# Optimization experiments

Measured on AMD Instinct MI355X. Metric: run time of the kernel, lower is better.

## Reference

```python
import jax, jax.numpy as jnp
import numpy as np

# ---- constants from module defaults ----
IMG, PS, STRIDE, C_IN = 224, 16, 8, 1
NP1D = (IMG - PS) // STRIDE + 1          # 27
NUM_PATCHES = NP1D * NP1D                # 729
EMBED = 64
N_INPUT = NUM_PATCHES * EMBED            # 46656
N_HIDDEN = 1000                          # d_model
N_RNN = 100
N_STEPS = 5
BETA, THR = 0.8, 0.5
BETA_R, THR_R = 0.95, 1.0
LM_SPN = 0.0058
ALPHA = 2.0  # snntorch ATan surrogate default

@jax.custom_vjp
def spike(x):
    return (x > 0).astype(x.dtype)

def _spike_fwd(x):
    return spike(x), x

def _spike_bwd(x, g):
    # snntorch ATan surrogate gradient
    return (g * (ALPHA / 2.0) / (1.0 + (jnp.pi / 2.0 * ALPHA * x) ** 2),)

spike.defvjp(_spike_fwd, _spike_bwd)

def extract_patches(x):
    # x: [B, C, H, W] -> [B, num_patches, C*PS*PS] matching torch unfold+permute+flatten
    B, C, H, W = x.shape
    idx = (jnp.arange(NP1D)[:, None] * STRIDE + jnp.arange(PS)).reshape(-1)  # [NP1D*PS]
    t = x[:, :, idx, :].reshape(B, C, NP1D, PS, W)
    t = t[..., idx].reshape(B, C, NP1D, PS, NP1D, PS)
    t = t.transpose(0, 2, 4, 1, 3, 5)  # [B, nh, nw, C, ph, pw]
    return t.reshape(B, NUM_PATCHES, C * PS * PS)

def setup_inputs() -> dict:
    key = jax.random.key(0)
    ks = jax.random.split(key, 12)
    def lin(k, fi, fo):
        kw, kb = jax.random.split(k)
        s = 1.0 / np.sqrt(fi)
        return (jax.random.uniform(kw, (fi, fo), jnp.float32, -s, s),
                jax.random.uniform(kb, (fo,), jnp.float32, -s, s))
    W_pe, b_pe = lin(ks[0], C_IN * PS * PS, EMBED)
    pos_embed = 0.02 * jax.random.normal(ks[1], (1, NUM_PATCHES, EMBED), jnp.float32)
    W1, b1 = lin(ks[2], N_INPUT, N_HIDDEN)
    W2, b2 = lin(ks[3], N_HIDDEN, N_HIDDEN)
    W3, b3 = lin(ks[4], N_HIDDEN, N_HIDDEN)
    WR, bR = lin(ks[5], N_HIDDEN, N_RNN)
    Vw, Vb = lin(ks[6], N_RNN, N_RNN)      # RLeaky recurrent linear
    Wq, bq = lin(ks[7], N_RNN, N_HIDDEN)
    Wk, bk = lin(ks[8], N_HIDDEN, N_HIDDEN)
    Wv, bv = lin(ks[9], N_HIDDEN, N_HIDDEN)
    Wo, bo = lin(ks[10], N_HIDDEN, 1)       # cross_last=True -> output_proj to 1
    data = jax.random.normal(ks[11], (32, C_IN, IMG, IMG), jnp.float32)
    return {"data": data, "W_pe": W_pe, "b_pe": b_pe, "pos_embed": pos_embed,
            "W1": W1, "b1": b1, "W2": W2, "b2": b2, "W3": W3, "b3": b3,
            "WR": WR, "bR": bR, "Vw": Vw, "Vb": Vb,
            "Wq": Wq, "bq": bq, "Wk": Wk, "bk": bk, "Wv": Wv, "bv": bv,
            "Wo": Wo, "bo": bo}

def _forward(data, W_pe, b_pe, pos_embed, W1, b1, W2, b2, W3, b3,
             WR, bR, Vw, Vb, Wq, bq, Wk, bk, Wv, bv, Wo, bo):
    B = data.shape[0]
    patches = extract_patches(data)                      # [B, 729, 256]
    x = patches @ W_pe + b_pe + pos_embed               # [B, 729, 64]
    x_flat = x.reshape(B, -1)                            # [B, 46656]
    cur1 = x_flat @ W1 + b1                              # constant across steps
    scale = jnp.sqrt(jnp.asarray(N_HIDDEN, jnp.float32))  # head_dim = d_model (1 head)

    def leaky(mem, cur, beta=BETA, thr=THR):
        reset = jax.lax.stop_gradient(spike(mem - thr))
        mem = beta * mem + cur - reset * thr
        return mem, spike(mem - thr)

    def step(carry, t):
        mem1, mem2, mem3, spk_r, mem_r, mem_out, total, prev, reg = carry
        # layers[:2] call -- first Leaky1 update
        mem1, spk1 = leaky(mem1, cur1)
        # layers[:7] call -- Leaky1 state updated a SECOND time (same x_flat)
        mem1, spk1b = leaky(mem1, cur1)
        mem2, spk2 = leaky(mem2, spk1b @ W2 + b2)
        mem3, spk3 = leaky(mem3, spk2 @ W3 + b3)  # Dropout is identity in eval
        total = total + spk1.mean() + spk3.mean()
        # RLeaky (beta=0.95, threshold=1.0, subtract reset, recurrent linear)
        rlin = spk1 @ WR + bR
        reset_r = jax.lax.stop_gradient(spike(mem_r - THR_R))
        mem_r = BETA_R * mem_r + rlin + spk_r @ Vw + Vb - reset_r * THR_R
        spk_r = spike(mem_r - THR_R)
        total = total + spk_r.mean()
        # cross-attention: feature dim acts as the sequence dim (seq=1 in view)
        q = spk_r @ Wq + bq                               # [B, 1000]
        k = spk3 @ Wk + bk                                # [B, 1000]
        v = spk3 @ Wv + bv                                # [B, 1000]
        probs = jax.nn.softmax(q[:, :, None] * k[:, None, :] / scale, axis=-1)  # [B,1000,1000]
        att = jnp.einsum('bij,bj->bi', probs, v) @ Wo + bo  # [B, 1]
        mem_out, spk_out = leaky(mem_out, att)
        mem_out = jax.lax.stop_gradient(mem_out)          # .detach() in source
        total = total + spk_out.mean()
        reg = reg + LM_SPN * total + jnp.where(t > 0, LM_SPN * jnp.abs(total - prev), 0.0)
        return (mem1, mem2, mem3, spk_r, mem_r, mem_out, total, total, reg), spk_out

    z = jnp.float32(0.0)
    init = (jnp.zeros((B, N_HIDDEN)), jnp.zeros((B, N_HIDDEN)), jnp.zeros((B, N_HIDDEN)),
            jnp.zeros((B, N_RNN)), jnp.zeros((B, N_RNN)), jnp.zeros((B, 1)), z, z, z)
    carry, spk_rec = jax.lax.scan(step, init, jnp.arange(N_STEPS))
    out = spk_rec.sum(0)[:, 0] / N_STEPS                  # [B]
    reg_norm = carry[-1] / N_STEPS
    return out, reg_norm

def reference(data, W_pe, b_pe, pos_embed, W1, b1, W2, b2, W3, b3,
              WR, bR, Vw, Vb, Wq, bq, Wk, bk, Wv, bv, Wo, bo):
    return _forward(data, W_pe, b_pe, pos_embed, W1, b1, W2, b2, W3, b3,
                    WR, bR, Vw, Vb, Wq, bq, Wk, bk, Wv, bv, Wo, bo)
```

## Files before the change

### kernel.cpp

```cpp
#include <hip/hip_runtime.h>

#define OFF_X     0
#define OFF_CUR1  1492992
#define OFF_MEM1  1524992
#define OFF_MEM2  1556992
#define OFF_MEM3  1588992
#define OFF_SPK1B 1652992
#define OFF_MEMR  1844992
#define OFF_SPKR  1848192
#define OFF_MEMO  1851392
#define OFF_PATT  1851424
#define OFF_CNT   1851680
#define OFF_OACC  1851700
#define OFF_SC    1851732
#define OFF_TICK  1851736
#define OFF_PART  1851744
#define OFF_PG2   OFF_PART
#define OFF_PG3   (OFF_PART + 800000)
#define OFF_PKK   (OFF_PART + 1600000)
#define OFF_PVV   (OFF_PART + 2400000)
#define OFF_M2B   (OFF_PART + 3200000)
#define OFF_M3B   (OFF_PART + 3232000)

static constexpr float kBETA  = 0.8f;
static constexpr float kTHR   = 0.5f;
static constexpr float kBETAR = 0.95f;
static constexpr float kTHRR  = 1.0f;
static constexpr float kLM    = 0.0058f;

__global__ void k_init(float* ws) {
    int idx = blockIdx.x * 256 + threadIdx.x;
    if (idx < 96000) {
        ws[OFF_MEM1 + idx] = 0.f;
    } else {
        int j = idx - 96000;
        if (j < 6752) ws[OFF_MEMR + j] = 0.f;
    }
}

__global__ __launch_bounds__(64) void k_patch(
    const float* __restrict__ data, const float* __restrict__ Wpe,
    const float* __restrict__ bpe, const float* __restrict__ pos,
    float* __restrict__ xf)
{
    int b = blockIdx.x, pr = blockIdx.y;
    int tid = threadIdx.x;
    const float* db = data + (size_t)b * 50176 + pr * 1792;
    float bb = bpe[tid];
    float acc[27];
    #pragma unroll
    for (int pc = 0; pc < 27; ++pc)
        acc[pc] = bb + pos[(pr * 27 + pc) * 64 + tid];
    #pragma unroll 2
    for (int c = 0; c < 256; ++c) {
        float w = Wpe[c * 64 + tid];
        const float* row = db + (c >> 4) * 224 + (c & 15);
        #pragma unroll
        for (int pc = 0; pc < 27; ++pc)
            acc[pc] = fmaf(row[pc * 8], w, acc[pc]);
    }
    size_t obase = (size_t)b * 46656 + (size_t)pr * 27 * 64 + tid;
    #pragma unroll
    for (int pc = 0; pc < 27; ++pc)
        xf[obase + (size_t)pc * 64] = acc[pc];
}

__global__ __launch_bounds__(256) void k_gemm1_part(
    const float* __restrict__ xf, const float* __restrict__ W1,
    float* __restrict__ part, int tpc)
{
    int chunk = blockIdx.x;
    int hg = blockIdx.y;
    int t0 = chunk * tpc;
    int t1 = t0 + tpc; if (t1 > 729) t1 = 729;
    int tid = threadIdx.x;
    __shared__ float xs[2048];
    float acc[32][2];
    #pragma unroll
    for (int b = 0; b < 32; ++b) { acc[b][0] = 0.f; acc[b][1] = 0.f; }

    const int hbase = hg * 500;
    const bool ok1 = (tid + 256) < 500;
    const int h0 = hbase + tid;
    const int h1 = hbase + (ok1 ? tid + 256 : 0);
    for (int tt = t0; tt < t1; ++tt) {
        int i0 = tt * 64;
        __syncthreads();
        for (int l = tid; l < 2048; l += 256)
            xs[l] = xf[(size_t)(l >> 6) * 46656 + i0 + (l & 63)];
        __syncthreads();
        for (int ii4 = 0; ii4 < 16; ++ii4) {
            int i = i0 + ii4 * 4;
            const float* c0 = W1 + (size_t)i * 1000 + h0;
            const float* c1 = W1 + (size_t)i * 1000 + h1;
            float w0a = c0[0], w1a = c0[1000], w2a = c0[2000], w3a = c0[3000];
            float w0b = ok1 ? c1[0]    : 0.f;
            float w1b = ok1 ? c1[1000] : 0.f;
            float w2b = ok1 ? c1[2000] : 0.f;
            float w3b = ok1 ? c1[3000] : 0.f;
            #pragma unroll
            for (int b = 0; b < 32; ++b) {
                float4 xv = *reinterpret_cast<const float4*>(&xs[b * 64 + ii4 * 4]);
                float a0 = acc[b][0], a1 = acc[b][1];
                a0 = fmaf(xv.x, w0a, a0);  a1 = fmaf(xv.x, w0b, a1);
                a0 = fmaf(xv.y, w1a, a0);  a1 = fmaf(xv.y, w1b, a1);
                a0 = fmaf(xv.z, w2a, a0);  a1 = fmaf(xv.z, w2b, a1);
                a0 = fmaf(xv.w, w3a, a0);  a1 = fmaf(xv.w, w3b, a1);
                acc[b][0] = a0; acc[b][1] = a1;
            }
        }
    }
    float* pc = part + (size_t)chunk * 32000 + hbase;
    #pragma unroll
    for (int b = 0; b < 32; ++b) {
        pc[b * 1000 + tid] = acc[b][0];
        if (ok1) pc[b * 1000 + tid + 256] = acc[b][1];
    }
}

__global__ void k_gemm1_reduce(const float* __restrict__ part,
                               const float* __restrict__ b1,
                               float* __restrict__ cur1, int nchunk)
{
    int idx = blockIdx.x * 128 + threadIdx.x;
    if (idx >= 32000) return;
    int h = idx % 1000;
    float a0 = b1[h], a1 = 0.f, a2 = 0.f, a3 = 0.f;
    int c = 0;
    for (; c + 4 <= nchunk; c += 4) {
        a0 += part[(size_t)c * 32000 + idx];
        a1 += part[(size_t)(c + 1) * 32000 + idx];
        a2 += part[(size_t)(c + 2) * 32000 + idx];
        a3 += part[(size_t)(c + 3) * 32000 + idx];
    }
    for (; c < nchunk; ++c) a0 += part[(size_t)c * 32000 + idx];
    cur1[idx] = (a0 + a1) + (a2 + a3);
}

__global__ __launch_bounds__(512) void k_stepR(
    const float* __restrict__ cur1, float* __restrict__ mem1,
    float* __restrict__ spk1b,
    const float* __restrict__ WR, const float* __restrict__ bR,
    const float* __restrict__ Vw, const float* __restrict__ Vb,
    float* __restrict__ mem_r, float* __restrict__ spk_r,
    float* cnt0, float* cnt2)
{
    int b = blockIdx.x;
    int tid = threadIdx.x;
    __shared__ float s1[1000];
    __shared__ float sr[100];
    __shared__ float red2[4][128];
    __shared__ float csum[8];

    float localc = 0.f;
    if (tid < 250) {
        int base = b * 1000 + tid * 4;
        float4 m4 = *reinterpret_cast<const float4*>(&mem1[base]);
        float4 c4 = *reinterpret_cast<const float4*>(&cur1[base]);
        float mm[4] = {m4.x, m4.y, m4.z, m4.w};
        float cc[4] = {c4.x, c4.y, c4.z, c4.w};
        float mb[4], sb[4];
        #pragma unroll
        for (int q = 0; q < 4; ++q) {
            float m = mm[q], c = cc[q];
            float r1 = (m - kTHR > 0.f) ? kTHR : 0.f;
            float ma = __fsub_rn(__fadd_rn(__fmul_rn(kBETA, m), c), r1);
            float s  = (ma - kTHR > 0.f) ? 1.f : 0.f;
            float r2 = __fmul_rn(s, kTHR);
            float mv = __fsub_rn(__fadd_rn(__fmul_rn(kBETA, ma), c), r2);
            sb[q] = (mv - kTHR > 0.f) ? 1.f : 0.f;
            mb[q] = mv;
            s1[tid * 4 + q] = s;
            localc += s;
        }
        *reinterpret_cast<float4*>(&mem1[base])  = make_float4(mb[0], mb[1], mb[2], mb[3]);
        *reinterpret_cast<float4*>(&spk1b[base]) = make_float4(sb[0], sb[1], sb[2], sb[3]);
    }
    if (tid < 100) sr[tid] = spk_r[b * 100 + tid];
    for (int off = 32; off; off >>= 1) localc += __shfl_down(localc, off, 64);
    if ((tid & 63) == 0) csum[tid >> 6] = localc;
    __syncthreads();
    if (tid == 0) {
        float cs = 0.f;
        #pragma unroll
        for (int w = 0; w < 8; ++w) cs += csum[w];
        atomicAdd(cnt0, cs);
    }

    int ks = tid >> 7, hh = tid & 127;
    float p = 0.f;
    if (hh < 100) {
        const float* wp = WR + (size_t)(ks * 250) * 100 + hh;
        int j0 = ks * 250;
        #pragma unroll 5
        for (int j = 0; j < 250; ++j) p = fmaf(s1[j0 + j], wp[(size_t)j * 100], p);
    }
    red2[ks][hh] = p;
    __syncthreads();
    float s = 0.f;
    if (tid < 100) {
        float acc = bR[tid] + ((red2[0][tid] + red2[1][tid]) + (red2[2][tid] + red2[3][tid]));
        float rec = 0.f;
        for (int j = 0; j < 100; ++j) rec = fmaf(sr[j], Vw[j * 100 + tid], rec);
        float m = mem_r[b * 100 + tid];
        float r = (m - kTHRR > 0.f) ? kTHRR : 0.f;
        float mn = __fsub_rn(__fadd_rn(__fadd_rn(__fadd_rn(__fmul_rn(kBETAR, m), acc), rec), Vb[tid]), r);
        s = (mn - kTHRR > 0.f) ? 1.f : 0.f;
        mem_r[b * 100 + tid] = mn;
        spk_r[b * 100 + tid] = s;
    }
    unsigned long long msk = __ballot(s > 0.5f);
    if ((tid & 63) == 0) {
        int pc2 = __popcll(msk);
        if (pc2) atomicAdd(cnt2, (float)pc2);
    }
}

__global__ __launch_bounds__(256) void k_gsp(
    const float* __restrict__ A, const float* __restrict__ W,
    float* __restrict__ part)
{
    int hb = blockIdx.x, kc = blockIdx.y, bg = blockIdx.z;
    int tid = threadIdx.x;
    int j0 = kc * 40;
    __shared__ __align__(16) float al[320];
    __shared__ float redg[8 * 128];
    for (int l = tid; l < 320; l += 256)
        al[l] = A[(size_t)(bg * 8 + (l & 7)) * 1000 + j0 + (l >> 3)];
    __syncthreads();
    int ks = tid >> 7, hh = tid & 127;
    float acc[8];
    #pragma unroll
    for (int b = 0; b < 8; ++b) acc[b] = 0.f;
    if (hh < 125) {
        int h = hb * 125 + hh;
        const float* Wp = W + (size_t)(j0 + ks * 20) * 1000 + h;
        const float4* abase = reinterpret_cast<const float4*>(&al[ks * 20 * 8]);
        #pragma unroll 4
        for (int jj = 0; jj < 20; ++jj) {
            float w = Wp[(size_t)jj * 1000];
            const float4* a4 = abase + jj * 2;
            #pragma unroll
            for (int q = 0; q < 2; ++q) {
                float4 av = a4[q];
                acc[q * 4 + 0] = fmaf(av.x, w, acc[q * 4 + 0]);
                acc[q * 4 + 1] = fmaf(av.y, w, acc[q * 4 + 1]);
                acc[q * 4 + 2] = fmaf(av.z, w, acc[q * 4 + 2]);
                acc[q * 4 + 3] = fmaf(av.w, w, acc[q * 4 + 3]);
            }
        }
    }
    if (ks == 1 && hh < 125) {
        #pragma unroll
        for (int b = 0; b < 8; ++b) redg[b * 128 + hh] = acc[b];
    }
    __syncthreads();
    if (ks == 0 && hh < 125) {
        int h = hb * 125 + hh;
        float* pp = part + (size_t)kc * 32000 + (size_t)(bg * 8) * 1000 + h;
        #pragma unroll
        for (int b = 0; b < 8; ++b) pp[(size_t)b * 1000] = acc[b] + redg[b * 128 + hh];
    }
}

template <bool COUNT>
__global__ __launch_bounds__(256) void k_gspred(
    const float* __restrict__ pin, const float* __restrict__ bias,
    const float* __restrict__ mem_old, float* __restrict__ mem_new,
    const float* __restrict__ W, float* __restrict__ pout, float* cnt)
{
    int hs = blockIdx.x, kc = blockIdx.y, bg = blockIdx.z;
    int tid = threadIdx.x;
    int j0 = kc * 40;
    __shared__ __align__(16) float al[320];
    __shared__ float redg[8 * 128];
    __shared__ float csum[4];
    float localc = 0.f;
    for (int e = tid; e < 320; e += 256) {
        int jj = e % 40, bi = e / 40;
        int idx = (bg * 8 + bi) * 1000 + j0 + jj;
        float a = bias[j0 + jj];
        #pragma unroll 5
        for (int c = 0; c < 25; ++c) a += pin[(size_t)c * 32000 + idx];
        float m = mem_old[idx];
        float r = (m - kTHR > 0.f) ? kTHR : 0.f;
        float mn = __fsub_rn(__fadd_rn(__fmul_rn(kBETA, m), a), r);
        float s = (mn - kTHR > 0.f) ? 1.f : 0.f;
        al[jj * 8 + bi] = s;
        if (hs == 0) { mem_new[idx] = mn; localc += s; }
    }
    if (COUNT) {
        for (int off = 32; off; off >>= 1) localc += __shfl_down(localc, off, 64);
        if ((tid & 63) == 0) csum[tid >> 6] = localc;
    }
    __syncthreads();
    if (COUNT && tid == 0 && hs == 0) {
        float tot = csum[0] + csum[1] + csum[2] + csum[3];
        if (tot != 0.f) atomicAdd(cnt, tot);
    }
    int ks = tid >> 7, hh = tid & 127;
    float acc[8];
    #pragma unroll
    for (int b = 0; b < 8; ++b) acc[b] = 0.f;
    if (hh < 125) {
        int h = hs * 125 + hh;
        const float* Wp = W + (size_t)(j0 + ks * 20) * 1000 + h;
        const float4* abase = reinterpret_cast<const float4*>(&al[ks * 20 * 8]);
        #pragma unroll 4
        for (int jj = 0; jj < 20; ++jj) {
            float w = Wp[(size_t)jj * 1000];
            const float4* a4 = abase + jj * 2;
            #pragma unroll
            for (int q = 0; q < 2; ++q) {
                float4 av = a4[q];
                acc[q * 4 + 0] = fmaf(av.x, w, acc[q * 4 + 0]);
                acc[q * 4 + 1] = fmaf(av.y, w, acc[q * 4 + 1]);
                acc[q * 4 + 2] = fmaf(av.z, w, acc[q * 4 + 2]);
                acc[q * 4 + 3] = fmaf(av.w, w, acc[q * 4 + 3]);
            }
        }
    }
    if (ks == 1 && hh < 125) {
        #pragma unroll
        for (int b = 0; b < 8; ++b) redg[b * 128 + hh] = acc[b];
    }
    __syncthreads();
    if (ks == 0 && hh < 125) {
        int h = hs * 125 + hh;
        float* pp = pout + (size_t)kc * 32000 + (size_t)(bg * 8) * 1000 + h;
        #pragma unroll
        for (int b = 0; b < 8; ++b) pp[(size_t)b * 1000] = acc[b] + redg[b * 128 + hh];
    }
}

__global__ __launch_bounds__(256) void k_gspred_kv(
    const float* __restrict__ pin, const float* __restrict__ bias,
    const float* __restrict__ mem_old, float* __restrict__ mem_new,
    const float* __restrict__ Wk, const float* __restrict__ Wv,
    float* __restrict__ pk, float* __restrict__ pv, float* cnt)
{
    int hs = blockIdx.x, kc = blockIdx.y, bg = blockIdx.z;
    int tid = threadIdx.x;
    int j0 = kc * 40;
    __shared__ __align__(16) float al[320];
    __shared__ float redk[8 * 128];
    __shared__ float redv[8 * 128];
    __shared__ float csum[4];
    float localc = 0.f;
    for (int e = tid; e < 320; e += 256) {
        int jj = e % 40, bi = e / 40;
        int idx = (bg * 8 + bi) * 1000 + j0 + jj;
        float a = bias[j0 + jj];
        #pragma unroll 5
        for (int c = 0; c < 25; ++c) a += pin[(size_t)c * 32000 + idx];
        float m = mem_old[idx];
        float r = (m - kTHR > 0.f) ? kTHR : 0.f;
        float mn = __fsub_rn(__fadd_rn(__fmul_rn(kBETA, m), a), r);
        float s = (mn - kTHR > 0.f) ? 1.f : 0.f;
        al[jj * 8 + bi] = s;
        if (hs == 0) { mem_new[idx] = mn; localc += s; }
    }
    for (int off = 32; off; off >>= 1) localc += __shfl_down(localc, off, 64);
    if ((tid & 63) == 0) csum[tid >> 6] = localc;
    __syncthreads();
    if (tid == 0 && hs == 0) {
        float tot = csum[0] + csum[1] + csum[2] + csum[3];
        if (tot != 0.f) atomicAdd(cnt, tot);
    }
    int ks = tid >> 7, hh = tid & 127;
    float ak[8], av2[8];
    #pragma unroll
    for (int b = 0; b < 8; ++b) { ak[b] = 0.f; av2[b] = 0.f; }
    if (hh < 125) {
        int h = hs * 125 + hh;
        const float* wkp = Wk + (size_t)(j0 + ks * 20) * 1000 + h;
        const float* wvp = Wv + (size_t)(j0 + ks * 20) * 1000 + h;
        const float4* abase = reinterpret_cast<const float4*>(&al[ks * 20 * 8]);
        #pragma unroll 4
        for (int jj = 0; jj < 20; ++jj) {
            float wk = wkp[(size_t)jj * 1000];
            float wv = wvp[(size_t)jj * 1000];
            const float4* a4 = abase + jj * 2;
            #pragma unroll
            for (int q = 0; q < 2; ++q) {
                float4 av = a4[q];
                ak[q * 4 + 0] = fmaf(av.x, wk, ak[q * 4 + 0]);
                ak[q * 4 + 1] = fmaf(av.y, wk, ak[q * 4 + 1]);
                ak[q * 4 + 2] = fmaf(av.z, wk, ak[q * 4 + 2]);
                ak[q * 4 + 3] = fmaf(av.w, wk, ak[q * 4 + 3]);
                av2[q * 4 + 0] = fmaf(av.x, wv, av2[q * 4 + 0]);
                av2[q * 4 + 1] = fmaf(av.y, wv, av2[q * 4 + 1]);
                av2[q * 4 + 2] = fmaf(av.z, wv, av2[q * 4 + 2]);
                av2[q * 4 + 3] = fmaf(av.w, wv, av2[q * 4 + 3]);
            }
        }
    }
    if (ks == 1 && hh < 125) {
        #pragma unroll
        for (int b = 0; b < 8; ++b) { redk[b * 128 + hh] = ak[b]; redv[b * 128 + hh] = av2[b]; }
    }
    __syncthreads();
    if (ks == 0 && hh < 125) {
        int h = hs * 125 + hh;
        float* ppk = pk + (size_t)kc * 32000 + (size_t)(bg * 8) * 1000 + h;
        float* ppv = pv + (size_t)kc * 32000 + (size_t)(bg * 8) * 1000 + h;
        #pragma unroll
        for (int b = 0; b < 8; ++b) {
            ppk[(size_t)b * 1000] = ak[b] + redk[b * 128 + hh];
            ppv[(size_t)b * 1000] = av2[b] + redv[b * 128 + hh];
        }
    }
}

__global__ __launch_bounds__(256) void k_attnred(
    const float* __restrict__ pkk, const float* __restrict__ pvv,
    const float* __restrict__ bk, const float* __restrict__ bv,
    const float* __restrict__ spkr, const float* __restrict__ Wq,
    const float* __restrict__ bq, const float* __restrict__ Wo,
    const float* __restrict__ bo,
    float* __restrict__ patt, float* __restrict__ memo,
    float* __restrict__ oacc, const float* __restrict__ cnt,
    float* __restrict__ sc, float* __restrict__ dout,
    unsigned int* __restrict__ tick, int t)
{
    int it = blockIdx.x, b = blockIdx.y;
    int tid = threadIdx.x;
    __shared__ float kk[1000], vv[1000];
    __shared__ float sr[100];
    __shared__ float red[256];
    __shared__ float pden[256], pnum[256];
    __shared__ int isLast;
    float pmax = -3.4e38f, pmin = 3.4e38f;
    if (tid < 100) sr[tid] = spkr[b * 100 + tid];
    for (int h = tid; h < 1000; h += 256) {
        int idx = b * 1000 + h;
        float ak = bk[h], av = bv[h];
        #pragma unroll 5
        for (int c = 0; c < 25; ++c) {
            ak += pkk[(size_t)c * 32000 + idx];
            av += pvv[(size_t)c * 32000 + idx];
        }
        kk[h] = ak; vv[h] = av;
        pmax = fmaxf(pmax, ak);
        pmin = fminf(pmin, ak);
    }
    red[tid] = pmax;
    __syncthreads();
    for (int s2 = 128; s2 > 0; s2 >>= 1) {
        if (tid < s2) red[tid] = fmaxf(red[tid], red[tid + s2]);
        __syncthreads();
    }
    float kmax = red[0];
    __syncthreads();
    red[tid] = pmin;
    __syncthreads();
    for (int s2 = 128; s2 > 0; s2 >>= 1) {
        if (tid < s2) red[tid] = fminf(red[tid], red[tid + s2]);
        __syncthreads();
    }
    float kmin = red[0];
    __syncthreads();

    int half = tid >> 7, lane = tid & 127;
    float den = 0.f, num = 0.f;
    if (lane < 125) {
        int i = it * 125 + lane;
        float qi = bq[i];
        for (int j = 0; j < 100; ++j) qi = fmaf(sr[j], Wq[j * 1000 + i], qi);
        float qs = qi / 31.62277660168379f;
        float m = (qs >= 0.f) ? qs * kmax : qs * kmin;
        int jb = half * 500;
        for (int j = 0; j < 500; ++j) {
            float e = __expf(fmaf(qs, kk[jb + j], -m));
            den += e;
            num = fmaf(e, vv[jb + j], num);
        }
    }
    pden[tid] = den; pnum[tid] = num;
    __syncthreads();
    float pw = 0.f;
    if (tid < 125) {
        float dsum = pden[tid] + pden[tid + 128];
        float nsum = pnum[tid] + pnum[tid + 128];
        pw = (nsum / dsum) * Wo[it * 125 + tid];
    }
    red[tid] = (tid < 125) ? pw : 0.f;
    __syncthreads();
    for (int s2 = 128; s2 > 0; s2 >>= 1) {
        if (tid < s2) red[tid] += red[tid + s2];
        __syncthreads();
    }
    if (tid == 0) patt[b * 8 + it] = red[0];
    __syncthreads();
    if (tid == 0) {
        __threadfence();
        unsigned r = atomicAdd(tick, 1u);
        isLast = (r == 255u) ? 1 : 0;
    }
    __syncthreads();
    if (isLast && tid < 64) {
        __threadfence();
        float s = 0.f;
        if (tid < 32) {
            float a = bo[0];
            for (int itx = 0; itx < 8; ++itx) a += patt[tid * 8 + itx];
            float m = memo[tid];
            float r = (m - kTHR > 0.f) ? kTHR : 0.f;
            float mn = __fsub_rn(__fadd_rn(__fmul_rn(kBETA, m), a), r);
            memo[tid] = mn;
            s = (mn - kTHR > 0.f) ? 1.f : 0.f;
            float oa = oacc[tid] + s;
            oacc[tid] = oa;
            if (t == 4) dout[tid] = oa / 5.0f;
        }
        unsigned long long msk = __ballot(s > 0.5f);
        float co = (float)__popcll(msk);
        if (tid == 0) {
            float total = sc[0];
            float prev = total;
            total = __fadd_rn(total, __fdiv_rn(cnt[0], 32000.f));
            total = __fadd_rn(total, __fdiv_rn(cnt[1], 32000.f));
            total = __fadd_rn(total, __fdiv_rn(cnt[2], 3200.f));
            total = __fadd_rn(total, __fdiv_rn(co, 32.f));
            float reg = sc[1];
            reg = __fadd_rn(reg, __fmul_rn(kLM, total));
            if (t > 0) reg = __fadd_rn(reg, __fmul_rn(kLM, fabsf(__fsub_rn(total, prev))));
            sc[0] = total; sc[1] = reg;
            if (t == 4) dout[32] = reg / 5.0f;
        }
    }
}

extern "C" void kernel_launch(void* const* d_in, const int* in_sizes, int n_in,
                              void* d_out, int out_size, void* d_ws, size_t ws_size,
                              hipStream_t stream)
{
    const float* data = (const float*)d_in[0];
    const float* Wpe  = (const float*)d_in[1];
    const float* bpe  = (const float*)d_in[2];
    const float* pos  = (const float*)d_in[3];
    const float* W1   = (const float*)d_in[4];
    const float* b1   = (const float*)d_in[5];
    const float* W2   = (const float*)d_in[6];
    const float* b2   = (const float*)d_in[7];
    const float* W3   = (const float*)d_in[8];
    const float* b3   = (const float*)d_in[9];
    const float* WR   = (const float*)d_in[10];
    const float* bR   = (const float*)d_in[11];
    const float* Vw   = (const float*)d_in[12];
    const float* Vb   = (const float*)d_in[13];
    const float* Wq   = (const float*)d_in[14];
    const float* bq   = (const float*)d_in[15];
    const float* Wk   = (const float*)d_in[16];
    const float* bk   = (const float*)d_in[17];
    const float* Wv   = (const float*)d_in[18];
    const float* bv   = (const float*)d_in[19];
    const float* Wo   = (const float*)d_in[20];
    const float* bo   = (const float*)d_in[21];

    float* ws = (float*)d_ws;
    float* dout = (float*)d_out;

    float* xf    = ws + OFF_X;
    float* cur1  = ws + OFF_CUR1;
    float* mem1  = ws + OFF_MEM1;
    float* mem2a = ws + OFF_MEM2;
    float* mem3a = ws + OFF_MEM3;
    float* spk1b = ws + OFF_SPK1B;
    float* memr  = ws + OFF_MEMR;
    float* spkr  = ws + OFF_SPKR;
    float* memo  = ws + OFF_MEMO;
    float* patt  = ws + OFF_PATT;
    float* cntb  = ws + OFF_CNT;
    float* oacc  = ws + OFF_OACC;
    float* sc    = ws + OFF_SC;
    unsigned int* tick = (unsigned int*)(ws + OFF_TICK);
    float* part  = ws + OFF_PART;
    float* pg2   = ws + OFF_PG2;
    float* pg3   = ws + OFF_PG3;
    float* pkk   = ws + OFF_PKK;
    float* pvv   = ws + OFF_PVV;
    float* mem2b = ws + OFF_M2B;
    float* mem3b = ws + OFF_M3B;

    size_t ws_f = ws_size / 4;
    size_t avail = (ws_f > OFF_PART) ? (ws_f - OFF_PART) : 0;
    long nchunk_l = (long)(avail / 32000);
    int nchunk = (nchunk_l > 365) ? 365 : (int)nchunk_l;
    if (nchunk < 1) nchunk = 1;
    int tpc = (729 + nchunk - 1) / nchunk;
    nchunk = (729 + tpc - 1) / tpc;

    k_init<<<402, 256, 0, stream>>>(ws);
    k_patch<<<dim3(32, 27), 64, 0, stream>>>(data, Wpe, bpe, pos, xf);
    k_gemm1_part<<<dim3(nchunk, 2), 256, 0, stream>>>(xf, W1, part, tpc);
    k_gemm1_reduce<<<250, 128, 0, stream>>>(part, b1, cur1, nchunk);

    for (int t = 0; t < 5; ++t) {
        float* cnt = cntb + t * 4;
        float* m2o = (t & 1) ? mem2b : mem2a;
        float* m2n = (t & 1) ? mem2a : mem2b;
        float* m3o = (t & 1) ? mem3b : mem3a;
        float* m3n = (t & 1) ? mem3a : mem3b;

        k_stepR<<<32, 512, 0, stream>>>(cur1, mem1, spk1b, WR, bR, Vw, Vb,
                                        memr, spkr, cnt + 0, cnt + 2);
        k_gsp<<<dim3(8, 25, 4), 256, 0, stream>>>(spk1b, W2, pg2);
        k_gspred<false><<<dim3(8, 25, 4), 256, 0, stream>>>(
            pg2, b2, m2o, m2n, W3, pg3, nullptr);
        k_gspred_kv<<<dim3(8, 25, 4), 256, 0, stream>>>(
            pg3, b3, m3o, m3n, Wk, Wv, pkk, pvv, cnt + 1);
        k_attnred<<<dim3(8, 32), 256, 0, stream>>>(
            pkk, pvv, bk, bv, spkr, Wq, bq, Wo, bo,
            patt, memo, oacc, cnt, sc, dout, tick + t, t);
    }
    (void)in_sizes; (void)n_in; (void)out_size;
}
```

Baseline: 545.1 us.

## Fold per-step leaky update and RNN layer into neighboring kernels to cut launches

Removes the separate k_stepR launch each timestep. The layer-1 membrane update for the next step now runs in extra blocks of k_attnred, with one initial k_stepA launch before the loop. The RLeaky recurrent layer runs in an extra block column of k_gsp. This trims five serial launches and lets small work overlap with the larger kernels. The cost is an extra spike buffer, added branch divergence and resource pressure in both host kernels, and a dependence on spk_r being read in k_attnred before k_gsp of the next step updates it.

```diff
diff --git a/kernel.cpp b/kernel.cpp
--- a/kernel.cpp
+++ b/kernel.cpp
@@ -21,6 +21,7 @@
 #define OFF_PVV   (OFF_PART + 2400000)
 #define OFF_M2B   (OFF_PART + 3200000)
 #define OFF_M3B   (OFF_PART + 3232000)
+#define OFF_SPK1  (OFF_PART + 3264000)
 
 static constexpr float kBETA  = 0.8f;
 static constexpr float kTHR   = 0.5f;
@@ -137,94 +138,87 @@
     cur1[idx] = (a0 + a1) + (a2 + a3);
 }
 
-__global__ __launch_bounds__(512) void k_stepR(
-    const float* __restrict__ cur1, float* __restrict__ mem1,
-    float* __restrict__ spk1b,
-    const float* __restrict__ WR, const float* __restrict__ bR,
-    const float* __restrict__ Vw, const float* __restrict__ Vb,
-    float* __restrict__ mem_r, float* __restrict__ spk_r,
-    float* cnt0, float* cnt2)
-{
-    int b = blockIdx.x;
-    int tid = threadIdx.x;
-    __shared__ float s1[1000];
-    __shared__ float sr[100];
-    __shared__ float red2[4][128];
-    __shared__ float csum[8];
-
-    float localc = 0.f;
-    if (tid < 250) {
-        int base = b * 1000 + tid * 4;
-        float4 m4 = *reinterpret_cast<const float4*>(&mem1[base]);
-        float4 c4 = *reinterpret_cast<const float4*>(&cur1[base]);
-        float mm[4] = {m4.x, m4.y, m4.z, m4.w};
-        float cc[4] = {c4.x, c4.y, c4.z, c4.w};
-        float mb[4], sb[4];
-        #pragma unroll
-        for (int q = 0; q < 4; ++q) {
-            float m = mm[q], c = cc[q];
-            float r1 = (m - kTHR > 0.f) ? kTHR : 0.f;
-            float ma = __fsub_rn(__fadd_rn(__fmul_rn(kBETA, m), c), r1);
-            float s  = (ma - kTHR > 0.f) ? 1.f : 0.f;
-            float r2 = __fmul_rn(s, kTHR);
-            float mv = __fsub_rn(__fadd_rn(__fmul_rn(kBETA, ma), c), r2);
-            sb[q] = (mv - kTHR > 0.f) ? 1.f : 0.f;
-            mb[q] = mv;
-            s1[tid * 4 + q] = s;
-            localc += s;
-        }
-        *reinterpret_cast<float4*>(&mem1[base])  = make_float4(mb[0], mb[1], mb[2], mb[3]);
-        *reinterpret_cast<float4*>(&spk1b[base]) = make_float4(sb[0], sb[1], sb[2], sb[3]);
-    }
-    if (tid < 100) sr[tid] = spk_r[b * 100 + tid];
-    for (int off = 32; off; off >>= 1) localc += __shfl_down(localc, off, 64);
-    if ((tid & 63) == 0) csum[tid >> 6] = localc;
-    __syncthreads();
-    if (tid == 0) {
-        float cs = 0.f;
-        #pragma unroll
-        for (int w = 0; w < 8; ++w) cs += csum[w];
-        atomicAdd(cnt0, cs);
-    }
-
-    int ks = tid >> 7, hh = tid & 127;
-    float p = 0.f;
-    if (hh < 100) {
-        const float* wp = WR + (size_t)(ks * 250) * 100 + hh;
-        int j0 = ks * 250;
-        #pragma unroll 5
-        for (int j = 0; j < 250; ++j) p = fmaf(s1[j0 + j], wp[(size_t)j * 100], p);
-    }
-    red2[ks][hh] = p;
-    __syncthreads();
-    float s = 0.f;
-    if (tid < 100) {
-        float acc = bR[tid] + ((red2[0][tid] + red2[1][tid]) + (red2[2][tid] + red2[3][tid]));
-        float rec = 0.f;
-        for (int j = 0; j < 100; ++j) rec = fmaf(sr[j], Vw[j * 100 + tid], rec);
-        float m = mem_r[b * 100 + tid];
-        float r = (m - kTHRR > 0.f) ? kTHRR : 0.f;
-        float mn = __fsub_rn(__fadd_rn(__fadd_rn(__fadd_rn(__fmul_rn(kBETAR, m), acc), rec), Vb[tid]), r);
-        s = (mn - kTHRR > 0.f) ? 1.f : 0.f;
-        mem_r[b * 100 + tid] = mn;
-        spk_r[b * 100 + tid] = s;
-    }
-    unsigned long long msk = __ballot(s > 0.5f);
-    if ((tid & 63) == 0) {
-        int pc2 = __popcll(msk);
-        if (pc2) atomicAdd(cnt2, (float)pc2);
+__device__ __forceinline__ void stepA_elem(
+    const float* cur1, float* mem1, float* spk1, float* spk1b,
+    int idx, float& s1v)
+{
+    float m = mem1[idx], c = cur1[idx];
+    float r1 = (m - kTHR > 0.f) ? kTHR : 0.f;
+    float ma = __fsub_rn(__fadd_rn(__fmul_rn(kBETA, m), c), r1);
+    s1v = (ma - kTHR > 0.f) ? 1.f : 0.f;
+    float r2 = __fmul_rn(s1v, kTHR);
+    float mb = __fsub_rn(__fadd_rn(__fmul_rn(kBETA, ma), c), r2);
+    float s1bv = (mb - kTHR > 0.f) ? 1.f : 0.f;
+    mem1[idx] = mb; spk1[idx] = s1v; spk1b[idx] = s1bv;
+}
+
+__global__ void k_stepA(const float* __restrict__ cur1, float* __restrict__ mem1,
+                        float* __restrict__ spk1, float* __restrict__ spk1b, float* cnt)
+{
+    int idx = blockIdx.x * 256 + threadIdx.x;
+    float s1v = 0.f;
+    if (idx < 32000)
+        stepA_elem(cur1, mem1, spk1, spk1b, idx, s1v);
+    unsigned long long msk = __ballot(s1v > 0.5f);
+    if ((threadIdx.x & 63) == 0) {
+        int p = __popcll(msk);
+        if (p) atomicAdd(cnt, (float)p);
     }
 }
 
 __global__ __launch_bounds__(256) void k_gsp(
     const float* __restrict__ A, const float* __restrict__ W,
-    float* __restrict__ part)
+    float* __restrict__ part,
+    const float* __restrict__ spk1, const float* __restrict__ WR,
+    const float* __restrict__ bR, const float* __restrict__ Vw,
+    const float* __restrict__ Vb, float* __restrict__ mem_r,
+    float* __restrict__ spk_r, float* cnt2)
 {
     int hb = blockIdx.x, kc = blockIdx.y, bg = blockIdx.z;
     int tid = threadIdx.x;
-    int j0 = kc * 40;
     __shared__ __align__(16) float al[320];
     __shared__ float redg[8 * 128];
+    __shared__ float s1l[1000];
+    __shared__ float srl[100];
+    __shared__ float red2l[256];
+
+    if (hb == 8) {
+        if (kc >= 8) return;
+        int b = kc * 4 + bg;
+        for (int l = tid; l < 1000; l += 256) s1l[l] = spk1[b * 1000 + l];
+        if (tid < 100) srl[tid] = spk_r[b * 100 + tid];
+        __syncthreads();
+        int ks = tid >> 7, hh = tid & 127;
+        float p = 0.f;
+        if (hh < 100) {
+            const float* wp = WR + (size_t)(ks * 500) * 100 + hh;
+            int j0r = ks * 500;
+            #pragma unroll 4
+            for (int j = 0; j < 500; ++j) p = fmaf(s1l[j0r + j], wp[(size_t)j * 100], p);
+        }
+        red2l[ks * 128 + hh] = p;
+        __syncthreads();
+        float s = 0.f;
+        if (tid < 100) {
+            float acc = bR[tid] + red2l[tid] + red2l[128 + tid];
+            float rec = 0.f;
+            for (int j = 0; j < 100; ++j) rec = fmaf(srl[j], Vw[j * 100 + tid], rec);
+            float m = mem_r[b * 100 + tid];
+            float r = (m - kTHRR > 0.f) ? kTHRR : 0.f;
+            float mn = __fsub_rn(__fadd_rn(__fadd_rn(__fadd_rn(__fmul_rn(kBETAR, m), acc), rec), Vb[tid]), r);
+            s = (mn - kTHRR > 0.f) ? 1.f : 0.f;
+            mem_r[b * 100 + tid] = mn;
+            spk_r[b * 100 + tid] = s;
+        }
+        unsigned long long msk = __ballot(s > 0.5f);
+        if ((tid & 63) == 0) {
+            int pc2 = __popcll(msk);
+            if (pc2) atomicAdd(cnt2, (float)pc2);
+        }
+        return;
+    }
+
+    int j0 = kc * 40;
     for (int l = tid; l < 320; l += 256)
         al[l] = A[(size_t)(bg * 8 + (l & 7)) * 1000 + j0 + (l >> 3)];
     __syncthreads();
@@ -421,10 +415,31 @@
     float* __restrict__ patt, float* __restrict__ memo,
     float* __restrict__ oacc, const float* __restrict__ cnt,
     float* __restrict__ sc, float* __restrict__ dout,
-    unsigned int* __restrict__ tick, int t)
+    unsigned int* __restrict__ tick, int t,
+    const float* __restrict__ cur1, float* __restrict__ mem1,
+    float* __restrict__ spk1, float* __restrict__ spk1b,
+    float* __restrict__ cnt_next)
 {
     int it = blockIdx.x, b = blockIdx.y;
     int tid = threadIdx.x;
+
+    if (it >= 8) {
+        if (t < 4) {
+            int sid = (it - 8) * 32 + b;
+            float s1v = 0.f;
+            if (tid < 250) {
+                int idx = sid * 250 + tid;
+                stepA_elem(cur1, mem1, spk1, spk1b, idx, s1v);
+            }
+            unsigned long long msk = __ballot(s1v > 0.5f);
+            if ((tid & 63) == 0) {
+                int p = __popcll(msk);
+                if (p) atomicAdd(cnt_next, (float)p);
+            }
+        }
+        return;
+    }
+
     __shared__ float kk[1000], vv[1000];
     __shared__ float sr[100];
     __shared__ float red[256];
@@ -582,6 +597,7 @@
     float* pvv   = ws + OFF_PVV;
     float* mem2b = ws + OFF_M2B;
     float* mem3b = ws + OFF_M3B;
+    float* spk1  = ws + OFF_SPK1;
 
     size_t ws_f = ws_size / 4;
     size_t avail = (ws_f > OFF_PART) ? (ws_f - OFF_PART) : 0;
@@ -595,6 +611,7 @@
     k_patch<<<dim3(32, 27), 64, 0, stream>>>(data, Wpe, bpe, pos, xf);
     k_gemm1_part<<<dim3(nchunk, 2), 256, 0, stream>>>(xf, W1, part, tpc);
     k_gemm1_reduce<<<250, 128, 0, stream>>>(part, b1, cur1, nchunk);
+    k_stepA<<<125, 256, 0, stream>>>(cur1, mem1, spk1, spk1b, cntb + 0);
 
     for (int t = 0; t < 5; ++t) {
         float* cnt = cntb + t * 4;
@@ -602,17 +619,18 @@
         float* m2n = (t & 1) ? mem2a : mem2b;
         float* m3o = (t & 1) ? mem3b : mem3a;
         float* m3n = (t & 1) ? mem3a : mem3b;
-
-        k_stepR<<<32, 512, 0, stream>>>(cur1, mem1, spk1b, WR, bR, Vw, Vb,
-                                        memr, spkr, cnt + 0, cnt + 2);
-        k_gsp<<<dim3(8, 25, 4), 256, 0, stream>>>(spk1b, W2, pg2);
+        float* cnt_next = (t < 4) ? (cntb + (t + 1) * 4) : cntb;
+
+        k_gsp<<<dim3(9, 25, 4), 256, 0, stream>>>(
+            spk1b, W2, pg2, spk1, WR, bR, Vw, Vb, memr, spkr, cnt + 2);
         k_gspred<false><<<dim3(8, 25, 4), 256, 0, stream>>>(
             pg2, b2, m2o, m2n, W3, pg3, nullptr);
         k_gspred_kv<<<dim3(8, 25, 4), 256, 0, stream>>>(
             pg3, b3, m3o, m3n, Wk, Wv, pkk, pvv, cnt + 1);
-        k_attnred<<<dim3(8, 32), 256, 0, stream>>>(
+        k_attnred<<<dim3(12, 32), 256, 0, stream>>>(
             pkk, pvv, bk, bv, spkr, Wq, bq, Wo, bo,
-            patt, memo, oacc, cnt, sc, dout, tick + t, t);
+            patt, memo, oacc, cnt, sc, dout, tick + t, t,
+            cur1, mem1, spk1, spk1b, cnt_next);
     }
     (void)in_sizes; (void)n_in; (void)out_size;
 }
```

Result: slower. 644.1 us (+18.2%).
